# Performance work log

Measured on AMD Instinct MI355X. Metric: run time of the kernel, lower is better.

## Reference

```python
import math
import jax, jax.numpy as jnp
import numpy as np

H = 512   # hidden_size
NH = 8    # num_heads
HD = H // NH  # per_head_size


def get_embedding(max_len, dim):
    # FLAT-style sinusoidal relative position embedding over positions [-L, L-1]
    half = dim // 2
    freq = jnp.exp(jnp.arange(half, dtype=jnp.float32) * (-math.log(10000.0) / (half - 1)))
    pos = jnp.arange(-max_len, max_len, dtype=jnp.float32)  # [2L]
    ang = pos[:, None] * freq[None, :]                      # [2L, half]
    return jnp.concatenate([jnp.sin(ang), jnp.cos(ang)], axis=1)  # [2L, dim]


def setup_inputs() -> dict:
    key = jax.random.key(0)
    ks = jax.random.split(key, 9)
    B, L = 4, 1024
    return {
        "query": jax.random.normal(ks[0], (B, L, H), jnp.float32),
        "key": jax.random.normal(ks[1], (B, L, H), jnp.float32),
        "value": jax.random.normal(ks[2], (B, L, H), jnp.float32),
        "w_q_w": jax.random.normal(ks[3], (H, H), jnp.float32) * 0.02,
        "w_q_b": jnp.zeros((H,), jnp.float32),
        "w_v_w": jax.random.normal(ks[4], (H, H), jnp.float32) * 0.02,
        "w_v_b": jnp.zeros((H,), jnp.float32),
        "w_r_w": jax.random.normal(ks[5], (H, HD), jnp.float32) * 0.02,
        "w_r_b": jnp.zeros((HD,), jnp.float32),
        "r_r_bias": jax.random.normal(ks[6], (NH, HD), jnp.float32) * 0.02,
        "r_w_bias": jax.random.normal(ks[7], (NH, HD), jnp.float32) * 0.02,
        "seq_len": 1000,
    }


def reference(query, key, value, w_q_w, w_q_b, w_v_w, w_v_b, w_r_w, w_r_b,
              r_r_bias, r_w_bias, seq_len):
    B, L, _ = key.shape
    # projections (torch Linear == x @ W + b with W stored as [in, out] here)
    q = (query @ w_q_w + w_q_b).reshape(B, L, NH, HD).transpose(0, 2, 1, 3)  # [B,N,L,D]
    v = (value @ w_v_w + w_v_b).reshape(B, L, NH, HD).transpose(0, 2, 1, 3)
    k = key.reshape(B, L, NH, HD).transpose(0, 2, 1, 3)

    rel = get_embedding(L, H) @ w_r_w + w_r_b  # [2L, HD], positions -L..L-1

    rw_head_q = q + r_r_bias[None, :, None, :]
    AC = jnp.einsum('bnqd,bnkd->bnqk', rw_head_q, k)                 # [B,N,L,L]
    D_ = jnp.einsum('nd,ld->nl', r_w_bias, rel)[None, :, None, :]    # [1,N,1,2L]
    B_ = jnp.einsum('bnqd,ld->bnql', q, rel)                         # [B,N,L,2L]
    E_ = jnp.einsum('bnkd,ld->bnkl', k, rel)                         # [B,N,L,2L]
    BD = B_ + D_

    # _shift:           out[q,k] = BD[q, L + k - q]
    # _transpose_shift: out[q,k] = E_[k, L + q - k]
    qi = jnp.arange(L)
    idx_bd = L + qi[None, :] - qi[:, None]                 # [L,L]: L+k-q
    BD_sh = BD[:, :, qi[:, None], idx_bd]                  # [B,N,L,L]
    rows_e = jnp.broadcast_to(qi[None, :], (L, L))         # [L,L]: k
    idx_e = L + qi[:, None] - qi[None, :]                  # [L,L]: L+q-k
    E_sh = E_[:, :, rows_e, idx_e]                         # [B,N,L,L]

    attn = AC + BD_sh + E_sh
    mask = (jnp.arange(L) < seq_len)[None, None, None, :]  # key mask
    attn = jnp.where(mask, attn, jnp.float32(-1e15))
    attn = jax.nn.softmax(attn, axis=-1)

    out = jnp.matmul(attn, v)                               # [B,N,L,D]
    return out.transpose(0, 2, 1, 3).reshape(B, L, H)
```

## Files before the change

### kernel.cpp

```cpp
#include <hip/hip_runtime.h>
#include <math.h>

#define HDIM  512
#define NHEAD 8
#define HEADD 64
#define BATCH 4
#define SEQ   1024
#define RELN  2048

typedef __attribute__((ext_vector_type(8))) short s16x8;
typedef __attribute__((ext_vector_type(4))) float f32x4;

__device__ __forceinline__ unsigned short f2bf(float x) {
    unsigned u = __float_as_uint(x);
    u += 0x7fffu + ((u >> 16) & 1u);
    return (unsigned short)(u >> 16);
}

__global__ void rel_kernel(const float* __restrict__ w_r_w,
                           const float* __restrict__ w_r_b,
                           unsigned short* __restrict__ relbf)
{
    __shared__ float emb_s[HDIM];
    const int l = blockIdx.x;
    const int d = threadIdx.x;
    const float pos  = (float)(l - SEQ);
    const float coef = (float)(-9.210340371976184 / 255.0);
    #pragma unroll
    for (int u = 0; u < 8; ++u) {
        int h  = u * 64 + d;
        int hh = (h < 256) ? h : (h - 256);
        float fr  = expf((float)hh * coef);
        float ang = pos * fr;
        emb_s[h] = (h < 256) ? sinf(ang) : cosf(ang);
    }
    __syncthreads();
    float acc = w_r_b[d];
    for (int h = 0; h < HDIM; ++h)
        acc = fmaf(emb_s[h], w_r_w[h * HEADD + d], acc);
    relbf[(size_t)l * HEADD + d] = f2bf(acc);
}

__global__ void conv_bf16(const float* __restrict__ in, unsigned short* __restrict__ out, int n)
{
    int i = (blockIdx.x * 256 + threadIdx.x) * 4;
    if (i < n) {
        float4 v = *(const float4*)(in + i);
        ushort4 o;
        o.x = f2bf(v.x); o.y = f2bf(v.y); o.z = f2bf(v.z); o.w = f2bf(v.w);
        *(ushort4*)(out + i) = o;
    }
}

__global__ __launch_bounds__(256) void proj_kernel(
    const float* __restrict__ A, const float* __restrict__ W,
    const float* __restrict__ bias,
    const float* __restrict__ extra1, const float* __restrict__ extra2,
    unsigned short* __restrict__ o1, unsigned short* __restrict__ o2)
{
    __shared__ float As[16][68];
    __shared__ float Bs[16][64];
    const int t  = threadIdx.x;
    const int m0 = blockIdx.y * 64;
    const int n0 = blockIdx.x * 64;
    const int tx = t & 15, ty = t >> 4;
    float acc[4][4] = {};
    for (int k0 = 0; k0 < HDIM; k0 += 16) {
        {
            int row = t >> 2, kq = (t & 3) * 4;
            float4 a4 = *(const float4*)(A + (size_t)(m0 + row) * HDIM + k0 + kq);
            As[kq + 0][row] = a4.x;
            As[kq + 1][row] = a4.y;
            As[kq + 2][row] = a4.z;
            As[kq + 3][row] = a4.w;
        }
        {
            int kk = t >> 4, nq = (t & 15) * 4;
            *(float4*)&Bs[kk][nq] = *(const float4*)(W + (size_t)(k0 + kk) * HDIM + n0 + nq);
        }
        __syncthreads();
        #pragma unroll
        for (int kk = 0; kk < 16; ++kk) {
            float4 a4 = *(const float4*)&As[kk][ty * 4];
            float4 b4 = *(const float4*)&Bs[kk][tx * 4];
            float av[4] = {a4.x, a4.y, a4.z, a4.w};
            float bv[4] = {b4.x, b4.y, b4.z, b4.w};
            #pragma unroll
            for (int mm = 0; mm < 4; ++mm)
                #pragma unroll
                for (int nn = 0; nn < 4; ++nn)
                    acc[mm][nn] = fmaf(av[mm], bv[nn], acc[mm][nn]);
        }
        __syncthreads();
    }
    #pragma unroll
    for (int mm = 0; mm < 4; ++mm) {
        int r  = m0 + ty * 4 + mm;
        int cc = n0 + tx * 4;
        float base[4];
        #pragma unroll
        for (int nn = 0; nn < 4; ++nn) base[nn] = acc[mm][nn] + bias[cc + nn];
        ushort4 pa;
        if (extra1) {
            pa.x = f2bf(base[0] + extra1[cc + 0]);
            pa.y = f2bf(base[1] + extra1[cc + 1]);
            pa.z = f2bf(base[2] + extra1[cc + 2]);
            pa.w = f2bf(base[3] + extra1[cc + 3]);
        } else {
            pa.x = f2bf(base[0]); pa.y = f2bf(base[1]);
            pa.z = f2bf(base[2]); pa.w = f2bf(base[3]);
        }
        *(ushort4*)(o1 + (size_t)r * HDIM + cc) = pa;
        if (o2) {
            ushort4 pb;
            pb.x = f2bf(base[0] + extra2[cc + 0]);
            pb.y = f2bf(base[1] + extra2[cc + 1]);
            pb.z = f2bf(base[2] + extra2[cc + 2]);
            pb.w = f2bf(base[3] + extra2[cc + 3]);
            *(ushort4*)(o2 + (size_t)r * HDIM + cc) = pb;
        }
    }
}

__global__ __launch_bounds__(256) void flash_mfma(
    const unsigned short* __restrict__ kbf,
    const unsigned short* __restrict__ qabf,
    const unsigned short* __restrict__ qbbf,
    const unsigned short* __restrict__ vbf,
    const unsigned short* __restrict__ relbf,
    const int* __restrict__ seqp,
    float* __restrict__ out)
{
    __shared__ unsigned short K_s[32][72];
    __shared__ unsigned short Vt_s[64][40];
    __shared__ unsigned short R2_s[64][72];
    __shared__ unsigned short R3_s[64][72];
    __shared__ float AC_s[32][36];
    __shared__ float M2_s[32][68];
    __shared__ float M3_s[32][68];
    __shared__ unsigned short P_s[32][32];
    __shared__ float scale_s[32];
    __shared__ float lsum_s[32];

    const int t  = threadIdx.x;
    const int w  = t >> 6;
    const int l  = t & 63;
    const int i0 = blockIdx.x * 32;
    const int n  = blockIdx.y;
    const int b  = blockIdx.z;
    const int S  = seqp[0];

    const int mi   = w >> 1;
    const int nq   = w & 1;
    const int colA = l & 15;
    const int g    = l >> 4;
    const int kg8  = g * 8;

    const int rq = i0 + mi * 16 + colA;
    const s16x8* qaP = (const s16x8*)(qabf + ((b * SEQ + rq) * HDIM + n * HEADD));
    const s16x8* qbP = (const s16x8*)(qbbf + ((b * SEQ + rq) * HDIM + n * HEADD));
    const s16x8 qa0 = qaP[g], qa1 = qaP[g + 4];
    const s16x8 qb0 = qbP[g], qb1 = qbP[g + 4];

    const int srow = t >> 3;
    const int sc8  = t & 7;

    float m_run = -1e30f, l_run = 0.0f;
    f32x4 o0 = {0.f, 0.f, 0.f, 0.f}, o1 = {0.f, 0.f, 0.f, 0.f};

    const int str  = t >> 3;
    const int std8 = (t & 7) * 8;

    for (int j0 = 0; j0 < S; j0 += 32) {
        {
            int gidx = (b * SEQ + j0 + str) * HDIM + n * HEADD + std8;
            *(uint4*)&K_s[str][std8] = *(const uint4*)(kbf + gidx);
            union { uint4 q; unsigned short s[8]; } vv;
            vv.q = *(const uint4*)(vbf + gidx);
            #pragma unroll
            for (int u = 0; u < 8; ++u) Vt_s[std8 + u][str] = vv.s[u];
        }
        {
            int base2 = SEQ + j0 - i0 - 31;
            int base3 = SEQ + i0 - j0 - 31;
            for (int u = t; u < 63 * 8; u += 256) {
                int rr = u >> 3, dd = (u & 7) * 8;
                *(uint4*)&R2_s[rr][dd] = *(const uint4*)(relbf + (base2 + rr) * HEADD + dd);
                *(uint4*)&R3_s[rr][dd] = *(const uint4*)(relbf + (base3 + rr) * HEADD + dd);
            }
        }
        __syncthreads();

        {
            f32x4 cAC = {0.f, 0.f, 0.f, 0.f};
            {
                int jb = nq * 16 + colA;
                s16x8 kb0 = *(const s16x8*)&K_s[jb][kg8];
                s16x8 kb1 = *(const s16x8*)&K_s[jb][kg8 + 32];
                cAC = __builtin_amdgcn_mfma_f32_16x16x32_bf16(qa0, kb0, cAC, 0, 0, 0);
                cAC = __builtin_amdgcn_mfma_f32_16x16x32_bf16(qa1, kb1, cAC, 0, 0, 0);
            }
            #pragma unroll
            for (int rr = 0; rr < 4; ++rr)
                AC_s[mi * 16 + g * 4 + rr][nq * 16 + colA] = cAC[rr];

            #pragma unroll
            for (int half = 0; half < 2; ++half) {
                int ni = nq * 2 + half;
                int u  = ni * 16 + colA;
                f32x4 c2 = {0.f, 0.f, 0.f, 0.f};
                s16x8 rb0 = *(const s16x8*)&R2_s[u][kg8];
                s16x8 rb1 = *(const s16x8*)&R2_s[u][kg8 + 32];
                c2 = __builtin_amdgcn_mfma_f32_16x16x32_bf16(qb0, rb0, c2, 0, 0, 0);
                c2 = __builtin_amdgcn_mfma_f32_16x16x32_bf16(qb1, rb1, c2, 0, 0, 0);
                #pragma unroll
                for (int rr = 0; rr < 4; ++rr)
                    M2_s[mi * 16 + g * 4 + rr][ni * 16 + colA] = c2[rr];
            }

            s16x8 ka0 = *(const s16x8*)&K_s[mi * 16 + colA][kg8];
            s16x8 ka1 = *(const s16x8*)&K_s[mi * 16 + colA][kg8 + 32];
            #pragma unroll
            for (int half = 0; half < 2; ++half) {
                int ni = nq * 2 + half;
                int u  = ni * 16 + colA;
                f32x4 c3 = {0.f, 0.f, 0.f, 0.f};
                s16x8 rb0 = *(const s16x8*)&R3_s[u][kg8];
                s16x8 rb1 = *(const s16x8*)&R3_s[u][kg8 + 32];
                c3 = __builtin_amdgcn_mfma_f32_16x16x32_bf16(ka0, rb0, c3, 0, 0, 0);
                c3 = __builtin_amdgcn_mfma_f32_16x16x32_bf16(ka1, rb1, c3, 0, 0, 0);
                #pragma unroll
                for (int rr = 0; rr < 4; ++rr)
                    M3_s[mi * 16 + g * 4 + rr][ni * 16 + colA] = c3[rr];
            }
        }
        __syncthreads();

        {
            f32x4 ac = *(const f32x4*)&AC_s[srow][sc8 * 4];
            float sv[4];
            #pragma unroll
            for (int u = 0; u < 4; ++u) {
                int col = sc8 * 4 + u;
                float s2 = M2_s[srow][col - srow + 31];
                float s3 = M3_s[col][srow - col + 31];
                float s  = ac[u] + s2 + s3;
                sv[u] = ((j0 + col) < S) ? s : -1e30f;
            }
            float mloc = fmaxf(fmaxf(sv[0], sv[1]), fmaxf(sv[2], sv[3]));
            #pragma unroll
            for (int off = 1; off < 8; off <<= 1)
                mloc = fmaxf(mloc, __shfl_xor(mloc, off));
            float mnew = fmaxf(m_run, mloc);
            float sc = exp2f((m_run - mnew) * 1.4426950408889634f);
            float p[4], ps;
            #pragma unroll
            for (int u = 0; u < 4; ++u)
                p[u] = exp2f((sv[u] - mnew) * 1.4426950408889634f);
            ps = p[0] + p[1] + p[2] + p[3];
            #pragma unroll
            for (int off = 1; off < 8; off <<= 1)
                ps += __shfl_xor(ps, off);
            l_run = l_run * sc + ps;
            m_run = mnew;
            ushort4 pk;
            pk.x = f2bf(p[0]); pk.y = f2bf(p[1]); pk.z = f2bf(p[2]); pk.w = f2bf(p[3]);
            *(ushort4*)&P_s[srow][sc8 * 4] = pk;
            if (sc8 == 0) scale_s[srow] = sc;
        }
        __syncthreads();

        {
            #pragma unroll
            for (int rr = 0; rr < 4; ++rr) {
                float scl = scale_s[mi * 16 + g * 4 + rr];
                o0[rr] *= scl;
                o1[rr] *= scl;
            }
            s16x8 pa  = *(const s16x8*)&P_s[mi * 16 + colA][kg8];
            s16x8 vb0 = *(const s16x8*)&Vt_s[nq * 16 + colA][kg8];
            s16x8 vb1 = *(const s16x8*)&Vt_s[nq * 16 + 32 + colA][kg8];
            o0 = __builtin_amdgcn_mfma_f32_16x16x32_bf16(pa, vb0, o0, 0, 0, 0);
            o1 = __builtin_amdgcn_mfma_f32_16x16x32_bf16(pa, vb1, o1, 0, 0, 0);
        }
        __syncthreads();
    }

    if (sc8 == 0) lsum_s[srow] = l_run;
    __syncthreads();

    #pragma unroll
    for (int rr = 0; rr < 4; ++rr) {
        int row = mi * 16 + g * 4 + rr;
        float inv = 1.0f / lsum_s[row];
        int obase = (b * SEQ + i0 + row) * HDIM + n * HEADD;
        out[obase + nq * 16 + colA]      = o0[rr] * inv;
        out[obase + nq * 16 + 32 + colA] = o1[rr] * inv;
    }
}

extern "C" void kernel_launch(void* const* d_in, const int* in_sizes, int n_in,
                              void* d_out, int out_size, void* d_ws, size_t ws_size,
                              hipStream_t stream) {
    (void)in_sizes; (void)n_in; (void)out_size; (void)ws_size;
    const float* query = (const float*)d_in[0];
    const float* key   = (const float*)d_in[1];
    const float* value = (const float*)d_in[2];
    const float* w_q_w = (const float*)d_in[3];
    const float* w_q_b = (const float*)d_in[4];
    const float* w_v_w = (const float*)d_in[5];
    const float* w_v_b = (const float*)d_in[6];
    const float* w_r_w = (const float*)d_in[7];
    const float* w_r_b = (const float*)d_in[8];
    const float* rrb   = (const float*)d_in[9];
    const float* rwb   = (const float*)d_in[10];
    const int*   seqp  = (const int*)d_in[11];
    float* out = (float*)d_out;

    unsigned short* wsp   = (unsigned short*)d_ws;
    unsigned short* relbf = wsp;
    unsigned short* kbf   = relbf + (size_t)RELN * HEADD;
    unsigned short* qabf  = kbf  + (size_t)BATCH * SEQ * HDIM;
    unsigned short* qbbf  = qabf + (size_t)BATCH * SEQ * HDIM;
    unsigned short* vbf   = qbbf + (size_t)BATCH * SEQ * HDIM;

    hipLaunchKernelGGL(rel_kernel, dim3(RELN), dim3(64), 0, stream, w_r_w, w_r_b, relbf);
    hipLaunchKernelGGL(conv_bf16, dim3(2048), dim3(256), 0, stream,
                       key, kbf, BATCH * SEQ * HDIM);
    hipLaunchKernelGGL(proj_kernel, dim3(8, 64), dim3(256), 0, stream,
                       query, w_q_w, w_q_b, rrb, rwb, qabf, qbbf);
    hipLaunchKernelGGL(proj_kernel, dim3(8, 64), dim3(256), 0, stream,
                       value, w_v_w, w_v_b, (const float*)nullptr, (const float*)nullptr,
                       vbf, (unsigned short*)nullptr);
    hipLaunchKernelGGL(flash_mfma, dim3(SEQ / 32, NHEAD, BATCH), dim3(256), 0, stream,
                       kbf, qabf, qbbf, vbf, relbf, seqp, out);
}
```

Baseline: 301.4 us.

## Move projections to split-bf16 MFMA, pre-transpose V, restructure flash kernel

Replaces the FP32 SIMT projection GEMMs with MFMA GEMMs that split the activations and the pre-transposed weights into bf16 hi/lo parts (three MFMAs per tile) to keep near-FP32 accuracy. The V projection now writes a head-transposed layout so the attention kernel loads V tiles with vector stores instead of scalar transposes. The rel-embedding kernel is widened to 256 threads with a split-K reduction. The flash kernel is restructured: it uses swizzled rel tiles, stores the shift matrices in bf16 transposed, and runs the softmax in only two waves with per-row state. This adds a weight-split prep kernel and extra workspace, and the bf16 intermediates for the shift terms may cost some accuracy.

```diff
diff --git a/kernel.cpp b/kernel.cpp
--- a/kernel.cpp
+++ b/kernel.cpp
@@ -7,6 +7,7 @@
 #define BATCH 4
 #define SEQ   1024
 #define RELN  2048
+#define LOG2E 1.4426950408889634f
 
 typedef __attribute__((ext_vector_type(8))) short s16x8;
 typedef __attribute__((ext_vector_type(4))) float f32x4;
@@ -16,29 +17,78 @@
     u += 0x7fffu + ((u >> 16) & 1u);
     return (unsigned short)(u >> 16);
 }
-
-__global__ void rel_kernel(const float* __restrict__ w_r_w,
-                           const float* __restrict__ w_r_b,
-                           unsigned short* __restrict__ relbf)
+__device__ __forceinline__ float bf2f(unsigned short h) {
+    return __uint_as_float(((unsigned)h) << 16);
+}
+
+__global__ __launch_bounds__(256) void rel_kernel(const float* __restrict__ w_r_w,
+                                                  const float* __restrict__ w_r_b,
+                                                  unsigned short* __restrict__ relbf)
 {
     __shared__ float emb_s[HDIM];
+    __shared__ float part[4][64];
     const int l = blockIdx.x;
-    const int d = threadIdx.x;
+    const int t = threadIdx.x;
     const float pos  = (float)(l - SEQ);
     const float coef = (float)(-9.210340371976184 / 255.0);
+    {
+        float fr  = expf((float)t * coef);
+        float ang = pos * fr;
+        emb_s[t]       = sinf(ang);
+        emb_s[t + 256] = cosf(ang);
+    }
+    __syncthreads();
+    const int d  = t & 63;
+    const int ks = t >> 6;
+    const float* wp = w_r_w + d;
+    const int h0 = ks * 128;
+    float a0 = 0.f, a1 = 0.f, a2 = 0.f, a3 = 0.f;
+    #pragma unroll 8
+    for (int h = 0; h < 128; h += 4) {
+        a0 = fmaf(emb_s[h0 + h + 0], wp[(size_t)(h0 + h + 0) * HEADD], a0);
+        a1 = fmaf(emb_s[h0 + h + 1], wp[(size_t)(h0 + h + 1) * HEADD], a1);
+        a2 = fmaf(emb_s[h0 + h + 2], wp[(size_t)(h0 + h + 2) * HEADD], a2);
+        a3 = fmaf(emb_s[h0 + h + 3], wp[(size_t)(h0 + h + 3) * HEADD], a3);
+    }
+    part[ks][d] = (a0 + a1) + (a2 + a3);
+    __syncthreads();
+    if (ks == 0) {
+        float acc = part[0][d] + part[1][d] + part[2][d] + part[3][d] + w_r_b[d];
+        relbf[(size_t)l * HEADD + d] = f2bf(acc);
+    }
+}
+
+__global__ __launch_bounds__(256) void wsplit_kernel(
+    const float* __restrict__ wq, const float* __restrict__ wv,
+    unsigned short* __restrict__ wtq_hi, unsigned short* __restrict__ wtq_lo,
+    unsigned short* __restrict__ wtv_hi, unsigned short* __restrict__ wtv_lo)
+{
+    __shared__ float T[64][68];
+    const float* W = blockIdx.z ? wv : wq;
+    unsigned short* Ohi = blockIdx.z ? wtv_hi : wtq_hi;
+    unsigned short* Olo = blockIdx.z ? wtv_lo : wtq_lo;
+    const int k0 = blockIdx.y * 64, n0 = blockIdx.x * 64;
+    const int t = threadIdx.x;
+    const int r = t >> 2, c16 = (t & 3) * 16;
     #pragma unroll
-    for (int u = 0; u < 8; ++u) {
-        int h  = u * 64 + d;
-        int hh = (h < 256) ? h : (h - 256);
-        float fr  = expf((float)hh * coef);
-        float ang = pos * fr;
-        emb_s[h] = (h < 256) ? sinf(ang) : cosf(ang);
+    for (int u = 0; u < 4; ++u) {
+        float4 v = *(const float4*)(W + (size_t)(k0 + r) * HDIM + n0 + c16 + u * 4);
+        *(float4*)&T[r][c16 + u * 4] = v;
     }
     __syncthreads();
-    float acc = w_r_b[d];
-    for (int h = 0; h < HDIM; ++h)
-        acc = fmaf(emb_s[h], w_r_w[h * HEADD + d], acc);
-    relbf[(size_t)l * HEADD + d] = f2bf(acc);
+    __align__(16) unsigned short hi[16], lo[16];
+    #pragma unroll
+    for (int u = 0; u < 16; ++u) {
+        float x = T[c16 + u][r];
+        unsigned short h = f2bf(x);
+        hi[u] = h;
+        lo[u] = f2bf(x - bf2f(h));
+    }
+    size_t base = (size_t)(n0 + r) * HDIM + k0 + c16;
+    *(uint4*)(Ohi + base)     = *(uint4*)&hi[0];
+    *(uint4*)(Ohi + base + 8) = *(uint4*)&hi[8];
+    *(uint4*)(Olo + base)     = *(uint4*)&lo[0];
+    *(uint4*)(Olo + base + 8) = *(uint4*)&lo[8];
 }
 
 __global__ void conv_bf16(const float* __restrict__ in, unsigned short* __restrict__ out, int n)
@@ -52,250 +102,303 @@
     }
 }
 
-__global__ __launch_bounds__(256) void proj_kernel(
-    const float* __restrict__ A, const float* __restrict__ W,
+template<int MODE>
+__global__ __launch_bounds__(256) void proj_mfma(
+    const float* __restrict__ A,
+    const unsigned short* __restrict__ Wt_hi,
+    const unsigned short* __restrict__ Wt_lo,
     const float* __restrict__ bias,
-    const float* __restrict__ extra1, const float* __restrict__ extra2,
-    unsigned short* __restrict__ o1, unsigned short* __restrict__ o2)
+    const float* __restrict__ e1,
+    const float* __restrict__ e2,
+    unsigned short* __restrict__ out1,
+    unsigned short* __restrict__ out2)
 {
-    __shared__ float As[16][68];
-    __shared__ float Bs[16][64];
-    const int t  = threadIdx.x;
-    const int m0 = blockIdx.y * 64;
-    const int n0 = blockIdx.x * 64;
-    const int tx = t & 15, ty = t >> 4;
-    float acc[4][4] = {};
-    for (int k0 = 0; k0 < HDIM; k0 += 16) {
-        {
-            int row = t >> 2, kq = (t & 3) * 4;
-            float4 a4 = *(const float4*)(A + (size_t)(m0 + row) * HDIM + k0 + kq);
-            As[kq + 0][row] = a4.x;
-            As[kq + 1][row] = a4.y;
-            As[kq + 2][row] = a4.z;
-            As[kq + 3][row] = a4.w;
-        }
-        {
-            int kk = t >> 4, nq = (t & 15) * 4;
-            *(float4*)&Bs[kk][nq] = *(const float4*)(W + (size_t)(k0 + kk) * HDIM + n0 + nq);
-        }
-        __syncthreads();
-        #pragma unroll
-        for (int kk = 0; kk < 16; ++kk) {
-            float4 a4 = *(const float4*)&As[kk][ty * 4];
-            float4 b4 = *(const float4*)&Bs[kk][tx * 4];
-            float av[4] = {a4.x, a4.y, a4.z, a4.w};
-            float bv[4] = {b4.x, b4.y, b4.z, b4.w};
-            #pragma unroll
-            for (int mm = 0; mm < 4; ++mm)
+    __shared__ unsigned short Ah[64][40], Al[64][40], Bh[64][40], Bl[64][40];
+    __shared__ unsigned short Ls[64][72];
+    const int t = threadIdx.x;
+    const int w = t >> 6, l = t & 63, colA = l & 15, g = l >> 4, kg8 = g * 8;
+    const int n0 = blockIdx.x * 64, m0 = blockIdx.y * 64;
+    const int mi = w >> 1, ni = w & 1;
+    const int sr = t >> 2, skc = (t & 3) * 8;
+    f32x4 acc[2][2] = {};
+
+    for (int k0 = 0; k0 < HDIM; k0 += 32) {
+        {
+            const float* ap = A + (size_t)(m0 + sr) * HDIM + k0 + skc;
+            float4 x0 = *(const float4*)ap;
+            float4 x1 = *(const float4*)(ap + 4);
+            float xv[8] = {x0.x, x0.y, x0.z, x0.w, x1.x, x1.y, x1.z, x1.w};
+            __align__(16) unsigned short hh[8], ll[8];
+            #pragma unroll
+            for (int u = 0; u < 8; ++u) {
+                unsigned short h = f2bf(xv[u]);
+                hh[u] = h;
+                ll[u] = f2bf(xv[u] - bf2f(h));
+            }
+            *(uint4*)&Ah[sr][skc] = *(uint4*)hh;
+            *(uint4*)&Al[sr][skc] = *(uint4*)ll;
+            *(uint4*)&Bh[sr][skc] = *(const uint4*)(Wt_hi + (size_t)(n0 + sr) * HDIM + k0 + skc);
+            *(uint4*)&Bl[sr][skc] = *(const uint4*)(Wt_lo + (size_t)(n0 + sr) * HDIM + k0 + skc);
+        }
+        __syncthreads();
+        s16x8 ah[2], al[2], bh[2], bl[2];
+        #pragma unroll
+        for (int mt = 0; mt < 2; ++mt) {
+            ah[mt] = *(const s16x8*)&Ah[mi * 32 + mt * 16 + colA][kg8];
+            al[mt] = *(const s16x8*)&Al[mi * 32 + mt * 16 + colA][kg8];
+        }
+        #pragma unroll
+        for (int nt = 0; nt < 2; ++nt) {
+            bh[nt] = *(const s16x8*)&Bh[ni * 32 + nt * 16 + colA][kg8];
+            bl[nt] = *(const s16x8*)&Bl[ni * 32 + nt * 16 + colA][kg8];
+        }
+        #pragma unroll
+        for (int mt = 0; mt < 2; ++mt)
+            #pragma unroll
+            for (int nt = 0; nt < 2; ++nt) {
+                acc[mt][nt] = __builtin_amdgcn_mfma_f32_16x16x32_bf16(al[mt], bh[nt], acc[mt][nt], 0, 0, 0);
+                acc[mt][nt] = __builtin_amdgcn_mfma_f32_16x16x32_bf16(ah[mt], bl[nt], acc[mt][nt], 0, 0, 0);
+                acc[mt][nt] = __builtin_amdgcn_mfma_f32_16x16x32_bf16(ah[mt], bh[nt], acc[mt][nt], 0, 0, 0);
+            }
+        __syncthreads();
+    }
+
+    float bv[2], ev1[2], ev2[2];
+    #pragma unroll
+    for (int nt = 0; nt < 2; ++nt) {
+        int gn = n0 + ni * 32 + nt * 16 + colA;
+        bv[nt] = bias[gn];
+        if (MODE == 0) { ev1[nt] = e1[gn]; ev2[nt] = e2[gn]; }
+    }
+
+    if (MODE == 0) {
+        #pragma unroll
+        for (int mt = 0; mt < 2; ++mt)
+            #pragma unroll
+            for (int nt = 0; nt < 2; ++nt)
                 #pragma unroll
-                for (int nn = 0; nn < 4; ++nn)
-                    acc[mm][nn] = fmaf(av[mm], bv[nn], acc[mm][nn]);
-        }
-        __syncthreads();
-    }
-    #pragma unroll
-    for (int mm = 0; mm < 4; ++mm) {
-        int r  = m0 + ty * 4 + mm;
-        int cc = n0 + tx * 4;
-        float base[4];
-        #pragma unroll
-        for (int nn = 0; nn < 4; ++nn) base[nn] = acc[mm][nn] + bias[cc + nn];
-        ushort4 pa;
-        if (extra1) {
-            pa.x = f2bf(base[0] + extra1[cc + 0]);
-            pa.y = f2bf(base[1] + extra1[cc + 1]);
-            pa.z = f2bf(base[2] + extra1[cc + 2]);
-            pa.w = f2bf(base[3] + extra1[cc + 3]);
-        } else {
-            pa.x = f2bf(base[0]); pa.y = f2bf(base[1]);
-            pa.z = f2bf(base[2]); pa.w = f2bf(base[3]);
-        }
-        *(ushort4*)(o1 + (size_t)r * HDIM + cc) = pa;
-        if (o2) {
-            ushort4 pb;
-            pb.x = f2bf(base[0] + extra2[cc + 0]);
-            pb.y = f2bf(base[1] + extra2[cc + 1]);
-            pb.z = f2bf(base[2] + extra2[cc + 2]);
-            pb.w = f2bf(base[3] + extra2[cc + 3]);
-            *(ushort4*)(o2 + (size_t)r * HDIM + cc) = pb;
-        }
-    }
-}
-
-__global__ __launch_bounds__(256) void flash_mfma(
+                for (int rr = 0; rr < 4; ++rr)
+                    Ls[mi * 32 + mt * 16 + g * 4 + rr][ni * 32 + nt * 16 + colA] =
+                        f2bf(acc[mt][nt][rr] + bv[nt] + ev1[nt]);
+        __syncthreads();
+        {
+            int r = t >> 2, c = (t & 3) * 16;
+            uint4 x0 = *(uint4*)&Ls[r][c];
+            uint4 x1 = *(uint4*)&Ls[r][c + 8];
+            *(uint4*)(out1 + (size_t)(m0 + r) * HDIM + n0 + c)     = x0;
+            *(uint4*)(out1 + (size_t)(m0 + r) * HDIM + n0 + c + 8) = x1;
+        }
+        __syncthreads();
+        #pragma unroll
+        for (int mt = 0; mt < 2; ++mt)
+            #pragma unroll
+            for (int nt = 0; nt < 2; ++nt)
+                #pragma unroll
+                for (int rr = 0; rr < 4; ++rr)
+                    Ls[mi * 32 + mt * 16 + g * 4 + rr][ni * 32 + nt * 16 + colA] =
+                        f2bf(acc[mt][nt][rr] + bv[nt] + ev2[nt]);
+        __syncthreads();
+        {
+            int r = t >> 2, c = (t & 3) * 16;
+            uint4 x0 = *(uint4*)&Ls[r][c];
+            uint4 x1 = *(uint4*)&Ls[r][c + 8];
+            *(uint4*)(out2 + (size_t)(m0 + r) * HDIM + n0 + c)     = x0;
+            *(uint4*)(out2 + (size_t)(m0 + r) * HDIM + n0 + c + 8) = x1;
+        }
+    } else {
+        #pragma unroll
+        for (int mt = 0; mt < 2; ++mt)
+            #pragma unroll
+            for (int nt = 0; nt < 2; ++nt)
+                #pragma unroll
+                for (int rr = 0; rr < 4; ++rr)
+                    Ls[ni * 32 + nt * 16 + colA][mi * 32 + mt * 16 + g * 4 + rr] =
+                        f2bf(acc[mt][nt][rr] + bv[nt]);
+        __syncthreads();
+        {
+            int dl = t >> 2, c = (t & 3) * 16;
+            int head = n0 >> 6;
+            int bb = m0 >> 10, j0 = m0 & 1023;
+            uint4 x0 = *(uint4*)&Ls[dl][c];
+            uint4 x1 = *(uint4*)&Ls[dl][c + 8];
+            size_t vbase = ((size_t)(bb * NHEAD + head) * HEADD + dl) * SEQ + j0 + c;
+            *(uint4*)(out1 + vbase)     = x0;
+            *(uint4*)(out1 + vbase + 8) = x1;
+        }
+    }
+}
+
+__global__ __launch_bounds__(256) void flash_v3(
     const unsigned short* __restrict__ kbf,
     const unsigned short* __restrict__ qabf,
     const unsigned short* __restrict__ qbbf,
-    const unsigned short* __restrict__ vbf,
+    const unsigned short* __restrict__ vT,
     const unsigned short* __restrict__ relbf,
     const int* __restrict__ seqp,
     float* __restrict__ out)
 {
     __shared__ unsigned short K_s[32][72];
     __shared__ unsigned short Vt_s[64][40];
-    __shared__ unsigned short R2_s[64][72];
-    __shared__ unsigned short R3_s[64][72];
-    __shared__ float AC_s[32][36];
-    __shared__ float M2_s[32][68];
-    __shared__ float M3_s[32][68];
-    __shared__ unsigned short P_s[32][32];
+    __shared__ unsigned short R2_s[64 * 64];
+    __shared__ unsigned short R3_s[64 * 64];
+    __shared__ unsigned short M2t_s[64][36];
+    __shared__ unsigned short M3t_s[64][36];
+    __shared__ unsigned short P_s[32][40];
     __shared__ float scale_s[32];
     __shared__ float lsum_s[32];
 
-    const int t  = threadIdx.x;
-    const int w  = t >> 6;
-    const int l  = t & 63;
+    const int t = threadIdx.x;
+    const int w = t >> 6, l = t & 63, colA = l & 15, g = l >> 4, kg8 = g * 8;
     const int i0 = blockIdx.x * 32;
-    const int n  = blockIdx.y;
-    const int b  = blockIdx.z;
-    const int S  = seqp[0];
-
-    const int mi   = w >> 1;
-    const int nq   = w & 1;
-    const int colA = l & 15;
-    const int g    = l >> 4;
-    const int kg8  = g * 8;
-
-    const int rq = i0 + mi * 16 + colA;
-    const s16x8* qaP = (const s16x8*)(qabf + ((b * SEQ + rq) * HDIM + n * HEADD));
-    const s16x8* qbP = (const s16x8*)(qbbf + ((b * SEQ + rq) * HDIM + n * HEADD));
+    const int n = blockIdx.y, b = blockIdx.z;
+    const int S = seqp[0];
+
+    const int qa_row = i0 + (w & 1) * 16 + colA;
+    const int qb_row = i0 + (w == 3 ? 16 : 0) + colA;
+    const s16x8* qaP = (const s16x8*)(qabf + ((size_t)(b * SEQ + qa_row) * HDIM + n * HEADD));
+    const s16x8* qbP = (const s16x8*)(qbbf + ((size_t)(b * SEQ + qb_row) * HDIM + n * HEADD));
     const s16x8 qa0 = qaP[g], qa1 = qaP[g + 4];
     const s16x8 qb0 = qbP[g], qb1 = qbP[g + 4];
 
-    const int srow = t >> 3;
-    const int sc8  = t & 7;
-
-    float m_run = -1e30f, l_run = 0.0f;
+    float m_run[4] = {-1e30f, -1e30f, -1e30f, -1e30f};
+    float l_run[4] = {0.f, 0.f, 0.f, 0.f};
     f32x4 o0 = {0.f, 0.f, 0.f, 0.f}, o1 = {0.f, 0.f, 0.f, 0.f};
 
-    const int str  = t >> 3;
-    const int std8 = (t & 7) * 8;
+    const int krow = t >> 3, kc8 = (t & 7) * 8;
+    const int vrow = t >> 2, vc8 = (t & 3) * 8;
+    const int orow = (w & 1) * 16;
+    const int od   = (w >> 1) * 32;
 
     for (int j0 = 0; j0 < S; j0 += 32) {
-        {
-            int gidx = (b * SEQ + j0 + str) * HDIM + n * HEADD + std8;
-            *(uint4*)&K_s[str][std8] = *(const uint4*)(kbf + gidx);
-            union { uint4 q; unsigned short s[8]; } vv;
-            vv.q = *(const uint4*)(vbf + gidx);
-            #pragma unroll
-            for (int u = 0; u < 8; ++u) Vt_s[std8 + u][str] = vv.s[u];
-        }
-        {
-            int base2 = SEQ + j0 - i0 - 31;
-            int base3 = SEQ + i0 - j0 - 31;
-            for (int u = t; u < 63 * 8; u += 256) {
-                int rr = u >> 3, dd = (u & 7) * 8;
-                *(uint4*)&R2_s[rr][dd] = *(const uint4*)(relbf + (base2 + rr) * HEADD + dd);
-                *(uint4*)&R3_s[rr][dd] = *(const uint4*)(relbf + (base3 + rr) * HEADD + dd);
-            }
-        }
-        __syncthreads();
-
-        {
-            f32x4 cAC = {0.f, 0.f, 0.f, 0.f};
-            {
-                int jb = nq * 16 + colA;
-                s16x8 kb0 = *(const s16x8*)&K_s[jb][kg8];
-                s16x8 kb1 = *(const s16x8*)&K_s[jb][kg8 + 32];
-                cAC = __builtin_amdgcn_mfma_f32_16x16x32_bf16(qa0, kb0, cAC, 0, 0, 0);
-                cAC = __builtin_amdgcn_mfma_f32_16x16x32_bf16(qa1, kb1, cAC, 0, 0, 0);
-            }
-            #pragma unroll
-            for (int rr = 0; rr < 4; ++rr)
-                AC_s[mi * 16 + g * 4 + rr][nq * 16 + colA] = cAC[rr];
-
-            #pragma unroll
-            for (int half = 0; half < 2; ++half) {
-                int ni = nq * 2 + half;
-                int u  = ni * 16 + colA;
-                f32x4 c2 = {0.f, 0.f, 0.f, 0.f};
-                s16x8 rb0 = *(const s16x8*)&R2_s[u][kg8];
-                s16x8 rb1 = *(const s16x8*)&R2_s[u][kg8 + 32];
+        *(uint4*)&K_s[krow][kc8] =
+            *(const uint4*)(kbf + ((size_t)(b * SEQ + j0 + krow) * HDIM + n * HEADD + kc8));
+        *(uint4*)&Vt_s[vrow][vc8] =
+            *(const uint4*)(vT + ((size_t)((b * NHEAD + n) * HEADD + vrow) * SEQ + j0 + vc8));
+        {
+            const int base2 = SEQ + j0 - i0 - 31;
+            const int base3 = SEQ + i0 - j0 - 31;
+            #pragma unroll
+            for (int rep = 0; rep < 2; ++rep) {
+                int idx = t + rep * 256;
+                if (idx < 63 * 8) {
+                    int rw = idx >> 3, cc = (idx & 7) * 8;
+                    unsigned swz = ((unsigned)(rw * 128 + cc * 2)) ^ (unsigned)((rw & 7) << 4);
+                    *(uint4*)((char*)R2_s + swz) =
+                        *(const uint4*)(relbf + (size_t)(base2 + rw) * HEADD + cc);
+                    *(uint4*)((char*)R3_s + swz) =
+                        *(const uint4*)(relbf + (size_t)(base3 + rw) * HEADD + cc);
+                }
+            }
+        }
+        __syncthreads();
+
+        f32x4 accS[2] = {};
+        if (w < 2) {
+            #pragma unroll
+            for (int ct = 0; ct < 2; ++ct) {
+                s16x8 kb0 = *(const s16x8*)&K_s[ct * 16 + colA][kg8];
+                s16x8 kb1 = *(const s16x8*)&K_s[ct * 16 + colA][kg8 + 32];
+                accS[ct] = __builtin_amdgcn_mfma_f32_16x16x32_bf16(qa0, kb0, accS[ct], 0, 0, 0);
+                accS[ct] = __builtin_amdgcn_mfma_f32_16x16x32_bf16(qa1, kb1, accS[ct], 0, 0, 0);
+            }
+        } else {
+            const int wr = w - 2;
+            s16x8 ka0 = *(const s16x8*)&K_s[wr * 16 + colA][kg8];
+            s16x8 ka1 = *(const s16x8*)&K_s[wr * 16 + colA][kg8 + 32];
+            #pragma unroll
+            for (int ut = 0; ut < 4; ++ut) {
+                int urow = ut * 16 + colA;
+                unsigned sw0 = ((unsigned)(urow * 128 + kg8 * 2)) ^ (unsigned)((urow & 7) << 4);
+                unsigned sw1 = ((unsigned)(urow * 128 + (kg8 + 32) * 2)) ^ (unsigned)((urow & 7) << 4);
+                s16x8 rb0 = *(const s16x8*)((char*)R2_s + sw0);
+                s16x8 rb1 = *(const s16x8*)((char*)R2_s + sw1);
+                f32x4 c2 = {};
                 c2 = __builtin_amdgcn_mfma_f32_16x16x32_bf16(qb0, rb0, c2, 0, 0, 0);
                 c2 = __builtin_amdgcn_mfma_f32_16x16x32_bf16(qb1, rb1, c2, 0, 0, 0);
+                ushort4 p2;
+                p2.x = f2bf(c2[0]); p2.y = f2bf(c2[1]); p2.z = f2bf(c2[2]); p2.w = f2bf(c2[3]);
+                *(ushort4*)&M2t_s[urow][wr * 16 + g * 4] = p2;
+                s16x8 sb0 = *(const s16x8*)((char*)R3_s + sw0);
+                s16x8 sb1 = *(const s16x8*)((char*)R3_s + sw1);
+                f32x4 c3 = {};
+                c3 = __builtin_amdgcn_mfma_f32_16x16x32_bf16(ka0, sb0, c3, 0, 0, 0);
+                c3 = __builtin_amdgcn_mfma_f32_16x16x32_bf16(ka1, sb1, c3, 0, 0, 0);
+                ushort4 p3;
+                p3.x = f2bf(c3[0]); p3.y = f2bf(c3[1]); p3.z = f2bf(c3[2]); p3.w = f2bf(c3[3]);
+                *(ushort4*)&M3t_s[urow][wr * 16 + g * 4] = p3;
+            }
+        }
+        __syncthreads();
+
+        if (w < 2) {
+            float sv[2][4];
+            #pragma unroll
+            for (int ct = 0; ct < 2; ++ct) {
+                int col = ct * 16 + colA;
+                bool ok = (j0 + col) < S;
                 #pragma unroll
-                for (int rr = 0; rr < 4; ++rr)
-                    M2_s[mi * 16 + g * 4 + rr][ni * 16 + colA] = c2[rr];
-            }
-
-            s16x8 ka0 = *(const s16x8*)&K_s[mi * 16 + colA][kg8];
-            s16x8 ka1 = *(const s16x8*)&K_s[mi * 16 + colA][kg8 + 32];
-            #pragma unroll
-            for (int half = 0; half < 2; ++half) {
-                int ni = nq * 2 + half;
-                int u  = ni * 16 + colA;
-                f32x4 c3 = {0.f, 0.f, 0.f, 0.f};
-                s16x8 rb0 = *(const s16x8*)&R3_s[u][kg8];
-                s16x8 rb1 = *(const s16x8*)&R3_s[u][kg8 + 32];
-                c3 = __builtin_amdgcn_mfma_f32_16x16x32_bf16(ka0, rb0, c3, 0, 0, 0);
-                c3 = __builtin_amdgcn_mfma_f32_16x16x32_bf16(ka1, rb1, c3, 0, 0, 0);
-                #pragma unroll
-                for (int rr = 0; rr < 4; ++rr)
-                    M3_s[mi * 16 + g * 4 + rr][ni * 16 + colA] = c3[rr];
-            }
-        }
-        __syncthreads();
-
-        {
-            f32x4 ac = *(const f32x4*)&AC_s[srow][sc8 * 4];
-            float sv[4];
-            #pragma unroll
-            for (int u = 0; u < 4; ++u) {
-                int col = sc8 * 4 + u;
-                float s2 = M2_s[srow][col - srow + 31];
-                float s3 = M3_s[col][srow - col + 31];
-                float s  = ac[u] + s2 + s3;
-                sv[u] = ((j0 + col) < S) ? s : -1e30f;
-            }
-            float mloc = fmaxf(fmaxf(sv[0], sv[1]), fmaxf(sv[2], sv[3]));
-            #pragma unroll
-            for (int off = 1; off < 8; off <<= 1)
-                mloc = fmaxf(mloc, __shfl_xor(mloc, off));
-            float mnew = fmaxf(m_run, mloc);
-            float sc = exp2f((m_run - mnew) * 1.4426950408889634f);
-            float p[4], ps;
-            #pragma unroll
-            for (int u = 0; u < 4; ++u)
-                p[u] = exp2f((sv[u] - mnew) * 1.4426950408889634f);
-            ps = p[0] + p[1] + p[2] + p[3];
-            #pragma unroll
-            for (int off = 1; off < 8; off <<= 1)
-                ps += __shfl_xor(ps, off);
-            l_run = l_run * sc + ps;
-            m_run = mnew;
-            ushort4 pk;
-            pk.x = f2bf(p[0]); pk.y = f2bf(p[1]); pk.z = f2bf(p[2]); pk.w = f2bf(p[3]);
-            *(ushort4*)&P_s[srow][sc8 * 4] = pk;
-            if (sc8 == 0) scale_s[srow] = sc;
-        }
-        __syncthreads();
-
-        {
+                for (int rr = 0; rr < 4; ++rr) {
+                    int grow = orow + g * 4 + rr;
+                    float s2 = bf2f(M2t_s[col - grow + 31][grow]);
+                    float s3 = bf2f(M3t_s[grow - col + 31][col]);
+                    float s = accS[ct][rr] + s2 + s3;
+                    sv[ct][rr] = ok ? s : -1e30f;
+                }
+            }
             #pragma unroll
             for (int rr = 0; rr < 4; ++rr) {
-                float scl = scale_s[mi * 16 + g * 4 + rr];
-                o0[rr] *= scl;
-                o1[rr] *= scl;
-            }
-            s16x8 pa  = *(const s16x8*)&P_s[mi * 16 + colA][kg8];
-            s16x8 vb0 = *(const s16x8*)&Vt_s[nq * 16 + colA][kg8];
-            s16x8 vb1 = *(const s16x8*)&Vt_s[nq * 16 + 32 + colA][kg8];
+                float mm = fmaxf(sv[0][rr], sv[1][rr]);
+                mm = fmaxf(mm, __shfl_xor(mm, 1));
+                mm = fmaxf(mm, __shfl_xor(mm, 2));
+                mm = fmaxf(mm, __shfl_xor(mm, 4));
+                mm = fmaxf(mm, __shfl_xor(mm, 8));
+                float mnew = fmaxf(m_run[rr], mm);
+                float sc = exp2f((m_run[rr] - mnew) * LOG2E);
+                m_run[rr] = mnew;
+                float p0 = exp2f((sv[0][rr] - mnew) * LOG2E);
+                float p1 = exp2f((sv[1][rr] - mnew) * LOG2E);
+                P_s[orow + g * 4 + rr][colA]      = f2bf(p0);
+                P_s[orow + g * 4 + rr][16 + colA] = f2bf(p1);
+                float pp = p0 + p1;
+                pp += __shfl_xor(pp, 1);
+                pp += __shfl_xor(pp, 2);
+                pp += __shfl_xor(pp, 4);
+                pp += __shfl_xor(pp, 8);
+                l_run[rr] = l_run[rr] * sc + pp;
+                if (colA == 0) scale_s[orow + g * 4 + rr] = sc;
+            }
+        }
+        __syncthreads();
+
+        {
+            float s0 = scale_s[orow + g * 4 + 0];
+            float s1 = scale_s[orow + g * 4 + 1];
+            float s2 = scale_s[orow + g * 4 + 2];
+            float s3 = scale_s[orow + g * 4 + 3];
+            o0[0] *= s0; o0[1] *= s1; o0[2] *= s2; o0[3] *= s3;
+            o1[0] *= s0; o1[1] *= s1; o1[2] *= s2; o1[3] *= s3;
+            s16x8 pa  = *(const s16x8*)&P_s[orow + colA][kg8];
+            s16x8 vb0 = *(const s16x8*)&Vt_s[od + colA][kg8];
+            s16x8 vb1 = *(const s16x8*)&Vt_s[od + 16 + colA][kg8];
             o0 = __builtin_amdgcn_mfma_f32_16x16x32_bf16(pa, vb0, o0, 0, 0, 0);
             o1 = __builtin_amdgcn_mfma_f32_16x16x32_bf16(pa, vb1, o1, 0, 0, 0);
         }
         __syncthreads();
     }
 
-    if (sc8 == 0) lsum_s[srow] = l_run;
+    if (w < 2 && colA == 0) {
+        #pragma unroll
+        for (int rr = 0; rr < 4; ++rr)
+            lsum_s[orow + g * 4 + rr] = l_run[rr];
+    }
     __syncthreads();
-
     #pragma unroll
     for (int rr = 0; rr < 4; ++rr) {
-        int row = mi * 16 + g * 4 + rr;
-        float inv = 1.0f / lsum_s[row];
-        int obase = (b * SEQ + i0 + row) * HDIM + n * HEADD;
-        out[obase + nq * 16 + colA]      = o0[rr] * inv;
-        out[obase + nq * 16 + 32 + colA] = o1[rr] * inv;
+        int row = orow + g * 4 + rr;
+        float inv = 1.f / lsum_s[row];
+        size_t obase = (size_t)(b * SEQ + i0 + row) * HDIM + n * HEADD;
+        out[obase + od + colA]      = o0[rr] * inv;
+        out[obase + od + 16 + colA] = o1[rr] * inv;
     }
 }
 
@@ -318,20 +421,27 @@
     float* out = (float*)d_out;
 
     unsigned short* wsp   = (unsigned short*)d_ws;
-    unsigned short* relbf = wsp;
-    unsigned short* kbf   = relbf + (size_t)RELN * HEADD;
-    unsigned short* qabf  = kbf  + (size_t)BATCH * SEQ * HDIM;
-    unsigned short* qbbf  = qabf + (size_t)BATCH * SEQ * HDIM;
-    unsigned short* vbf   = qbbf + (size_t)BATCH * SEQ * HDIM;
-
-    hipLaunchKernelGGL(rel_kernel, dim3(RELN), dim3(64), 0, stream, w_r_w, w_r_b, relbf);
+    const size_t NTOK = (size_t)BATCH * SEQ * HDIM;
+    unsigned short* relbf  = wsp;
+    unsigned short* kbf    = relbf + (size_t)RELN * HEADD;
+    unsigned short* qabf   = kbf + NTOK;
+    unsigned short* qbbf   = qabf + NTOK;
+    unsigned short* vTbuf  = qbbf + NTOK;
+    unsigned short* wtq_hi = vTbuf + NTOK;
+    unsigned short* wtq_lo = wtq_hi + (size_t)HDIM * HDIM;
+    unsigned short* wtv_hi = wtq_lo + (size_t)HDIM * HDIM;
+    unsigned short* wtv_lo = wtv_hi + (size_t)HDIM * HDIM;
+
+    hipLaunchKernelGGL(rel_kernel, dim3(RELN), dim3(256), 0, stream, w_r_w, w_r_b, relbf);
+    hipLaunchKernelGGL(wsplit_kernel, dim3(8, 8, 2), dim3(256), 0, stream,
+                       w_q_w, w_v_w, wtq_hi, wtq_lo, wtv_hi, wtv_lo);
     hipLaunchKernelGGL(conv_bf16, dim3(2048), dim3(256), 0, stream,
-                       key, kbf, BATCH * SEQ * HDIM);
-    hipLaunchKernelGGL(proj_kernel, dim3(8, 64), dim3(256), 0, stream,
-                       query, w_q_w, w_q_b, rrb, rwb, qabf, qbbf);
-    hipLaunchKernelGGL(proj_kernel, dim3(8, 64), dim3(256), 0, stream,
-                       value, w_v_w, w_v_b, (const float*)nullptr, (const float*)nullptr,
-                       vbf, (unsigned short*)nullptr);
-    hipLaunchKernelGGL(flash_mfma, dim3(SEQ / 32, NHEAD, BATCH), dim3(256), 0, stream,
-                       kbf, qabf, qbbf, vbf, relbf, seqp, out);
-}
+                       key, kbf, (int)NTOK);
+    hipLaunchKernelGGL((proj_mfma<0>), dim3(8, 64), dim3(256), 0, stream,
+                       query, wtq_hi, wtq_lo, w_q_b, rrb, rwb, qabf, qbbf);
+    hipLaunchKernelGGL((proj_mfma<1>), dim3(8, 64), dim3(256), 0, stream,
+                       value, wtv_hi, wtv_lo, w_v_b, (const float*)nullptr, (const float*)nullptr,
+                       vTbuf, (unsigned short*)nullptr);
+    hipLaunchKernelGGL(flash_v3, dim3(SEQ / 32, NHEAD, BATCH), dim3(256), 0, stream,
+                       kbf, qabf, qbbf, vTbuf, relbf, seqp, out);
+}
```

Result: faster. 252.9 us (-16.1%).
